# Optimization experiments

Hardware: AMD Instinct MI355X
Metric: run time of the kernel (lower is better)

Reference implementation:

```python
import jax, jax.numpy as jnp
import numpy as np

NEG_INF = -1e9  # matches torch masked_fill value of -1000000000.0


def setup_inputs() -> dict:
    key = jax.random.key(0)
    kq, kk, kv, km = jax.random.split(key, 4)
    B, H, L, D = 4, 16, 1024, 64
    query = jax.random.normal(kq, (B, H, L, D), dtype=jnp.float32)
    k_ = jax.random.normal(kk, (B, H, L, D), dtype=jnp.float32)
    value = jax.random.normal(kv, (B, H, L, D), dtype=jnp.float32)
    mask = jax.random.randint(km, (B, 1, L, L), 0, 2, dtype=jnp.int32)
    return {"query": query, "key": k_, "value": value, "mask": mask}


def reference(query, key, value, mask):
    # scores: [B, H, Lq, Lk]
    d = query.shape[-1]
    scores = jnp.einsum("bhqd,bhkd->bhqk", query, key) / jnp.sqrt(jnp.float32(d))
    masked = mask == 0  # broadcast [B,1,Lq,Lk] over heads
    scores = jnp.where(masked, jnp.float32(NEG_INF), scores)
    p_attn = jax.nn.softmax(scores, axis=-1)
    p_attn = jnp.where(masked, jnp.float32(0.0), p_attn)
    out = jnp.einsum("bhqk,bhkd->bhqd", p_attn, value)
    return out, p_attn
```

## Files before the change

### kernel.cpp

```cpp
#include <hip/hip_runtime.h>
#include <math.h>

typedef __attribute__((ext_vector_type(8))) short short8;
typedef __attribute__((ext_vector_type(4))) float f32x4;

#define NB 4
#define NH 16
#define SL 1024
#define DH 64
#define BQ 64
#define WQ 16
#define KTL 32
#define NT 256
#define NKT (SL / KTL)

#define TILE_SH (2 * KTL * DH)
#define HEAD_SH ((size_t)NKT * TILE_SH)
#define BLOB_SH ((size_t)NB * NH * HEAD_SH)
#define BMROW   (SL / 32)

#define QSCALE 0.18033688011111543f
#define NEGB  -1.5e9f

#if __has_builtin(__builtin_amdgcn_exp2f)
#define EXP2F(x) __builtin_amdgcn_exp2f(x)
#else
#define EXP2F(x) exp2f(x)
#endif

__device__ __forceinline__ unsigned short bf_rne(float x) {
    unsigned int u = __float_as_uint(x);
    u += 0x7fffu + ((u >> 16) & 1u);
    return (unsigned short)(u >> 16);
}
__device__ __forceinline__ void bf_split(float x, unsigned short& h, unsigned short& l) {
    unsigned int u = __float_as_uint(x);
    h = (unsigned short)(u >> 16);
    float r = x - __uint_as_float(u & 0xffff0000u);
    l = bf_rne(r);
}

typedef const __attribute__((address_space(1))) unsigned int guint_t;
typedef __attribute__((address_space(3))) unsigned int luint_t;
__device__ __forceinline__ void gload_lds16(const void* g, void* l) {
    __builtin_amdgcn_global_load_lds((guint_t*)g, (luint_t*)l, 16, 0, 0);
}

#define MFMA(a, b, c) __builtin_amdgcn_mfma_f32_16x16x32_bf16(a, b, c, 0, 0, 0)

#define WAITVM(N) do { asm volatile("s_waitcnt vmcnt(" #N ")" ::: "memory"); \
                       __builtin_amdgcn_sched_barrier(0); } while (0)
#define BAR() do { __builtin_amdgcn_sched_barrier(0); __builtin_amdgcn_s_barrier(); \
                   __builtin_amdgcn_sched_barrier(0); } while (0)
#define SCHED_FENCE() __builtin_amdgcn_sched_barrier(0)

__global__ __launch_bounds__(NT, 4) void prep_mask(
    const int* __restrict__ M, unsigned* __restrict__ bm)
{
    const size_t total = (size_t)NB * SL * SL;
    const int l = threadIdx.x & 63;
    for (size_t i = (size_t)blockIdx.x * NT + threadIdx.x; i < total;
         i += (size_t)gridDim.x * NT) {
        int v = M[i];
        unsigned long long b = __ballot(v != 0);
        if (l == 0)       bm[i >> 5] = (unsigned)b;
        else if (l == 32) bm[i >> 5] = (unsigned)(b >> 32);
    }
}

__global__ __launch_bounds__(NT, 4) void prep_split(
    const float* __restrict__ K, const float* __restrict__ V,
    unsigned short* __restrict__ kb, unsigned short* __restrict__ vb)
{
    __shared__ float sVs[KTL][DH + 4];

    const int t = threadIdx.x;
    const int kt = blockIdx.x, h = blockIdx.y, b = blockIdx.z;
    const size_t goff = (size_t)(b * NH + h) * SL * DH + (size_t)kt * KTL * DH;
    const size_t tks = (size_t)(b * NH + h) * HEAD_SH + (size_t)kt * TILE_SH;

    {
        int kr = t >> 3, c8 = t & 7;
        const float* src = K + goff + kr * DH + c8 * 8;
        float4 a = *(const float4*)src;
        float4 bb = *(const float4*)(src + 4);
        float vals[8] = {a.x, a.y, a.z, a.w, bb.x, bb.y, bb.z, bb.w};
        unsigned int ph[4], pl[4];
        #pragma unroll
        for (int j = 0; j < 4; ++j) {
            unsigned short h0, l0, h1, l1;
            bf_split(vals[2 * j], h0, l0);
            bf_split(vals[2 * j + 1], h1, l1);
            ph[j] = (unsigned int)h0 | ((unsigned int)h1 << 16);
            pl[j] = (unsigned int)l0 | ((unsigned int)l1 << 16);
        }
        int dsw = (c8 * 8) ^ ((kr & 7) << 3);
        *(uint4*)&kb[tks + kr * DH + dsw]           = make_uint4(ph[0], ph[1], ph[2], ph[3]);
        *(uint4*)&kb[tks + KTL * DH + kr * DH + dsw] = make_uint4(pl[0], pl[1], pl[2], pl[3]);
    }

    #pragma unroll
    for (int u = 0; u < 2; ++u) {
        int i = u * NT + t;
        float4 v = *(const float4*)(V + goff + (size_t)i * 4);
        *(float4*)&sVs[i >> 4][(i & 15) * 4] = v;
    }
    __syncthreads();
    {
        int d = t >> 2, k8 = t & 3;
        float vals[8];
        #pragma unroll
        for (int j = 0; j < 8; ++j) vals[j] = sVs[k8 * 8 + j][d];
        unsigned int ph[4], pl[4];
        #pragma unroll
        for (int j = 0; j < 4; ++j) {
            unsigned short h0, l0, h1, l1;
            bf_split(vals[2 * j], h0, l0);
            bf_split(vals[2 * j + 1], h1, l1);
            ph[j] = (unsigned int)h0 | ((unsigned int)h1 << 16);
            pl[j] = (unsigned int)l0 | ((unsigned int)l1 << 16);
        }
        int ksw = (k8 * 8) ^ ((d & 3) << 3);
        *(uint4*)&vb[tks + d * KTL + ksw]            = make_uint4(ph[0], ph[1], ph[2], ph[3]);
        *(uint4*)&vb[tks + KTL * DH + d * KTL + ksw] = make_uint4(pl[0], pl[1], pl[2], pl[3]);
    }
}

__global__ __launch_bounds__(NT, 4) void attn_main(
    const float* __restrict__ Q, const unsigned* __restrict__ bm,
    const unsigned short* __restrict__ kb, const unsigned short* __restrict__ vb,
    float* __restrict__ O, float* __restrict__ P)
{
    __shared__ unsigned short sK[2][TILE_SH];
    __shared__ unsigned short sV[2][TILE_SH];
    __shared__ unsigned short sPh[4][WQ][KTL];
    __shared__ unsigned short sPl[4][WQ][KTL];

    const int t = threadIdx.x;
    const int l = t & 63;
    const int w = __builtin_amdgcn_readfirstlane(t >> 6);
    const int lg = l >> 4, lr = l & 15;

    const int flat = blockIdx.x + (blockIdx.y << 4) + (blockIdx.z << 8);
    const int nid = (flat & 7) * 128 + (flat >> 3);
    const int qt = nid & 15;
    const int hh_ = (nid >> 4) & 15;
    const int b = nid >> 8;
    const int qb = qt * BQ + w * WQ;

    const size_t hoff = (size_t)(b * NH + hh_) * SL * DH;
    const size_t headsh = (size_t)(b * NH + hh_) * HEAD_SH;
    const unsigned short* kbh = kb + headsh;
    const unsigned short* vbh = vb + headsh;
    const unsigned* bmRow = bm + ((size_t)b * SL + qb + lr) * BMROW;
    float* Pw = P + ((size_t)(b * NH + hh_) * SL + qb) * SL;
    float* Ow = O + hoff + (size_t)qb * DH;

    short8 qhi[2], qlo[2];
    {
        const float* src0 = Q + hoff + (size_t)(qb + lr) * DH + lg * 8;
        #pragma unroll
        for (int ds = 0; ds < 2; ++ds) {
            const float* src = src0 + ds * 32;
            float4 a = *(const float4*)src;
            float4 bb = *(const float4*)(src + 4);
            float vals[8] = {a.x, a.y, a.z, a.w, bb.x, bb.y, bb.z, bb.w};
            #pragma unroll
            for (int j = 0; j < 8; ++j) {
                unsigned short hv, lv;
                bf_split(vals[j] * QSCALE, hv, lv);
                qhi[ds][j] = (short)hv;
                qlo[ds][j] = (short)lv;
            }
        }
    }

    auto stage = [&](unsigned short* lds, const unsigned short* gtile) {
        #pragma unroll
        for (int u = 0; u < 2; ++u) {
            const int c = w * 2 + u;
            gload_lds16((const char*)gtile + c * 1024 + l * 16, (char*)lds + c * 1024);
        }
    };

    stage(sK[0], kbh);
    unsigned bmv = bmRow[0];
    float m = -INFINITY, sum = 0.f;
    int cur = 0;

    for (int kt = 0; kt < NKT; ++kt) {
        WAITVM(0);
        BAR();
        unsigned bmn = 0;
        if (kt + 1 < NKT) {
            stage(sK[cur ^ 1], kbh + (size_t)(kt + 1) * TILE_SH);
            bmn = bmRow[kt + 1];
        }
        SCHED_FENCE();

        f32x4 acc[2];
        #pragma unroll
        for (int st = 0; st < 2; ++st) {
            const int krow = st * 16 + lr;
            const int sw = (krow & 7) << 3;
            f32x4 c = {0.f, 0.f, 0.f, 0.f};
            #pragma unroll
            for (int ds = 0; ds < 2; ++ds) {
                int dc = (ds * 32 + lg * 8) ^ sw;
                short8 ah = *(const short8*)&sK[cur][krow * DH + dc];
                short8 al = *(const short8*)&sK[cur][KTL * DH + krow * DH + dc];
                c = MFMA(ah, qhi[ds], c);
                c = MFMA(ah, qlo[ds], c);
                c = MFMA(al, qhi[ds], c);
            }
            acc[st] = c;
        }

        float s[8];
        #pragma unroll
        for (int st = 0; st < 2; ++st)
            #pragma unroll
            for (int j = 0; j < 4; ++j) {
                unsigned bit = (bmv >> (st * 16 + lg * 4 + j)) & 1u;
                s[st * 4 + j] = acc[st][j] + (bit ? 0.f : NEGB);
            }
        float tmax = s[0];
        #pragma unroll
        for (int j = 1; j < 8; ++j) tmax = fmaxf(tmax, s[j]);
        tmax = fmaxf(tmax, __shfl_xor(tmax, 16));
        tmax = fmaxf(tmax, __shfl_xor(tmax, 32));
        const float mn = fmaxf(m, tmax);
        float ts = 0.f;
        #pragma unroll
        for (int j = 0; j < 8; ++j) ts += EXP2F(s[j] - mn);
        ts += __shfl_xor(ts, 16);
        ts += __shfl_xor(ts, 32);
        sum = sum * EXP2F(m - mn) + ts;
        m = mn;
        bmv = bmn;
        cur ^= 1;
    }

    stage(sK[0], kbh);
    stage(sV[0], vbh);
    bmv = bmRow[0];
    const float m2 = m + __log2f(sum);
    f32x4 oacc[4];
    #pragma unroll
    for (int mt = 0; mt < 4; ++mt) oacc[mt] = (f32x4){0.f, 0.f, 0.f, 0.f};
    cur = 0;

    for (int kt = 0; kt < NKT; ++kt) {
        const int k0 = kt * KTL;
        if (kt == 0) { WAITVM(0); } else { WAITVM(2); }
        BAR();
        unsigned bmn = 0;
        if (kt + 1 < NKT) {
            stage(sK[cur ^ 1], kbh + (size_t)(kt + 1) * TILE_SH);
            stage(sV[cur ^ 1], vbh + (size_t)(kt + 1) * TILE_SH);
            bmn = bmRow[kt + 1];
        }
        SCHED_FENCE();

        f32x4 acc[2];
        #pragma unroll
        for (int st = 0; st < 2; ++st) {
            const int krow = st * 16 + lr;
            const int sw = (krow & 7) << 3;
            f32x4 c = {0.f, 0.f, 0.f, 0.f};
            #pragma unroll
            for (int ds = 0; ds < 2; ++ds) {
                int dc = (ds * 32 + lg * 8) ^ sw;
                short8 ah = *(const short8*)&sK[cur][krow * DH + dc];
                short8 al = *(const short8*)&sK[cur][KTL * DH + krow * DH + dc];
                c = MFMA(ah, qhi[ds], c);
                c = MFMA(ah, qlo[ds], c);
                c = MFMA(al, qhi[ds], c);
            }
            acc[st] = c;
        }

        #pragma unroll
        for (int st = 0; st < 2; ++st) {
            float p[4];
            #pragma unroll
            for (int j = 0; j < 4; ++j) {
                unsigned bit = (bmv >> (st * 16 + lg * 4 + j)) & 1u;
                float sj = acc[st][j] + (bit ? 0.f : NEGB);
                p[j] = EXP2F(sj - m2);
            }
            *(float4*)(Pw + (size_t)lr * SL + (k0 + st * 16 + lg * 4)) =
                make_float4(p[0], p[1], p[2], p[3]);
            unsigned short hv[4], lv[4];
            #pragma unroll
            for (int j = 0; j < 4; ++j) bf_split(p[j], hv[j], lv[j]);
            int col = (st * 16 + lg * 4) ^ ((lr & 3) << 3);
            uint2 uh, ul;
            uh.x = (unsigned int)hv[0] | ((unsigned int)hv[1] << 16);
            uh.y = (unsigned int)hv[2] | ((unsigned int)hv[3] << 16);
            ul.x = (unsigned int)lv[0] | ((unsigned int)lv[1] << 16);
            ul.y = (unsigned int)lv[2] | ((unsigned int)lv[3] << 16);
            *(uint2*)&sPh[w][lr][col] = uh;
            *(uint2*)&sPl[w][lr][col] = ul;
        }

        const int pcol = (lg * 8) ^ ((lr & 3) << 3);
        short8 pbh = *(const short8*)&sPh[w][lr][pcol];
        short8 pbl = *(const short8*)&sPl[w][lr][pcol];
        #pragma unroll
        for (int mt = 0; mt < 4; ++mt) {
            const int d = mt * 16 + lr;
            const int col = (lg * 8) ^ ((d & 3) << 3);
            short8 vh = *(const short8*)&sV[cur][d * KTL + col];
            short8 vl = *(const short8*)&sV[cur][KTL * DH + d * KTL + col];
            oacc[mt] = MFMA(vh, pbh, oacc[mt]);
            oacc[mt] = MFMA(vh, pbl, oacc[mt]);
            oacc[mt] = MFMA(vl, pbh, oacc[mt]);
        }
        bmv = bmn;
        cur ^= 1;
    }

    #pragma unroll
    for (int mt = 0; mt < 4; ++mt) {
        float4 o = make_float4(oacc[mt][0], oacc[mt][1], oacc[mt][2], oacc[mt][3]);
        *(float4*)(Ow + (size_t)lr * DH + mt * 16 + lg * 4) = o;
    }
}

__global__ __launch_bounds__(NT, 2) void attn_fallback(
    const float* __restrict__ Q, const float* __restrict__ K,
    const float* __restrict__ V, const int* __restrict__ M,
    float* __restrict__ O, float* __restrict__ P)
{
    __shared__ unsigned short sKhi[64][DH];
    __shared__ unsigned short sKlo[64][DH];
    __shared__ unsigned short sVhi[DH][64];
    __shared__ unsigned short sVlo[DH][64];
    __shared__ unsigned short sPhi[4][WQ][64];
    __shared__ unsigned short sPlo[4][WQ][64];

    const int t = threadIdx.x;
    const int l = t & 63;
    const int w = t >> 6;
    const int lg = l >> 4;
    const int lr = l & 15;

    const int hh_ = blockIdx.y, b = blockIdx.z;
    const int qb = blockIdx.x * BQ + w * WQ;

    const size_t hoff = (size_t)(b * NH + hh_) * SL * DH;
    const float* Kh = K + hoff;
    const float* Vh = V + hoff;
    const int*   Mw = M + ((size_t)b * SL + qb) * SL;
    float*       Pw = P + ((size_t)(b * NH + hh_) * SL + qb) * SL;
    float*       Ow = O + hoff + (size_t)qb * DH;

    short8 qhi[2], qlo[2];
    {
        const float* src0 = Q + hoff + (size_t)(qb + lr) * DH + lg * 8;
        #pragma unroll
        for (int ds = 0; ds < 2; ++ds) {
            const float* src = src0 + ds * 32;
            float4 a = *(const float4*)src;
            float4 bb = *(const float4*)(src + 4);
            float vals[8] = {a.x, a.y, a.z, a.w, bb.x, bb.y, bb.z, bb.w};
            #pragma unroll
            for (int j = 0; j < 8; ++j) {
                unsigned short hv, lv;
                bf_split(vals[j] * 0.125f, hv, lv);
                qhi[ds][j] = (short)hv;
                qlo[ds][j] = (short)lv;
            }
        }
    }

    auto stageK = [&](int k0) {
        #pragma unroll
        for (int u = 0; u < 2; ++u) {
            int idx = u * NT + t;
            int kr = idx >> 3;
            int dc = (idx & 7) * 8;
            const float* src = Kh + (size_t)(k0 + kr) * DH + dc;
            float4 a = *(const float4*)src;
            float4 bb = *(const float4*)(src + 4);
            float vals[8] = {a.x, a.y, a.z, a.w, bb.x, bb.y, bb.z, bb.w};
            unsigned int ph[4], pl[4];
            #pragma unroll
            for (int j = 0; j < 4; ++j) {
                unsigned short h0, l0, h1, l1;
                bf_split(vals[2 * j], h0, l0);
                bf_split(vals[2 * j + 1], h1, l1);
                ph[j] = (unsigned int)h0 | ((unsigned int)h1 << 16);
                pl[j] = (unsigned int)l0 | ((unsigned int)l1 << 16);
            }
            int dsw = dc ^ ((kr & 7) << 3);
            *(uint4*)&sKhi[kr][dsw] = make_uint4(ph[0], ph[1], ph[2], ph[3]);
            *(uint4*)&sKlo[kr][dsw] = make_uint4(pl[0], pl[1], pl[2], pl[3]);
        }
    };

    float m = -INFINITY, sum = 0.f;
    for (int kt = 0; kt < 16; ++kt) {
        const int k0 = kt * 64;
        __syncthreads();
        stageK(k0);
        __syncthreads();
        f32x4 acc[4];
        #pragma unroll
        for (int st = 0; st < 4; ++st) {
            const int krow = st * 16 + lr;
            const int sw = (krow & 7) << 3;
            f32x4 c = {0.f, 0.f, 0.f, 0.f};
            #pragma unroll
            for (int ds = 0; ds < 2; ++ds) {
                int dc = (ds * 32 + lg * 8) ^ sw;
                short8 ah = *(const short8*)&sKhi[krow][dc];
                short8 al = *(const short8*)&sKlo[krow][dc];
                c = MFMA(ah, qhi[ds], c);
                c = MFMA(ah, qlo[ds], c);
                c = MFMA(al, qhi[ds], c);
            }
            acc[st] = c;
        }
        float s[16];
        #pragma unroll
        for (int st = 0; st < 4; ++st) {
            const int4 mv = *(const int4*)(Mw + (size_t)lr * SL + k0 + st * 16 + lg * 4);
            s[st * 4 + 0] = mv.x ? acc[st][0] : -1e9f;
            s[st * 4 + 1] = mv.y ? acc[st][1] : -1e9f;
            s[st * 4 + 2] = mv.z ? acc[st][2] : -1e9f;
            s[st * 4 + 3] = mv.w ? acc[st][3] : -1e9f;
        }
        float tmax = s[0];
        #pragma unroll
        for (int j = 1; j < 16; ++j) tmax = fmaxf(tmax, s[j]);
        tmax = fmaxf(tmax, __shfl_xor(tmax, 16));
        tmax = fmaxf(tmax, __shfl_xor(tmax, 32));
        const float mn = fmaxf(m, tmax);
        float ts = 0.f;
        #pragma unroll
        for (int j = 0; j < 16; ++j) ts += __expf(s[j] - mn);
        ts += __shfl_xor(ts, 16);
        ts += __shfl_xor(ts, 32);
        sum = sum * __expf(m - mn) + ts;
        m = mn;
    }
    const float inv = 1.f / sum;

    f32x4 oacc[4];
    #pragma unroll
    for (int mt = 0; mt < 4; ++mt) oacc[mt] = (f32x4){0.f, 0.f, 0.f, 0.f};

    for (int kt = 0; kt < 16; ++kt) {
        const int k0 = kt * 64;
        __syncthreads();
        stageK(k0);
        {
            int d0 = (t & 15) * 4;
            int kl0 = (t >> 4) * 4;
            float4 r[4];
            #pragma unroll
            for (int i = 0; i < 4; ++i)
                r[i] = *(const float4*)(Vh + (size_t)(k0 + kl0 + i) * DH + d0);
            const float* rp = (const float*)r;
            #pragma unroll
            for (int j = 0; j < 4; ++j) {
                unsigned short hv[4], lv[4];
                #pragma unroll
                for (int i = 0; i < 4; ++i) bf_split(rp[i * 4 + j], hv[i], lv[i]);
                int d = d0 + j;
                int csw = kl0 ^ ((d & 7) << 3);
                uint2 uh, ul;
                uh.x = (unsigned int)hv[0] | ((unsigned int)hv[1] << 16);
                uh.y = (unsigned int)hv[2] | ((unsigned int)hv[3] << 16);
                ul.x = (unsigned int)lv[0] | ((unsigned int)lv[1] << 16);
                ul.y = (unsigned int)lv[2] | ((unsigned int)lv[3] << 16);
                *(uint2*)&sVhi[d][csw] = uh;
                *(uint2*)&sVlo[d][csw] = ul;
            }
        }
        __syncthreads();

        #pragma unroll
        for (int st = 0; st < 4; ++st) {
            const int krow = st * 16 + lr;
            const int sw = (krow & 7) << 3;
            f32x4 c = {0.f, 0.f, 0.f, 0.f};
            #pragma unroll
            for (int ds = 0; ds < 2; ++ds) {
                int dc = (ds * 32 + lg * 8) ^ sw;
                short8 ah = *(const short8*)&sKhi[krow][dc];
                short8 al = *(const short8*)&sKlo[krow][dc];
                c = MFMA(ah, qhi[ds], c);
                c = MFMA(ah, qlo[ds], c);
                c = MFMA(al, qhi[ds], c);
            }
            const int4 mv = *(const int4*)(Mw + (size_t)lr * SL + k0 + st * 16 + lg * 4);
            float p0 = mv.x ? __expf(c[0] - m) * inv : 0.f;
            float p1 = mv.y ? __expf(c[1] - m) * inv : 0.f;
            float p2 = mv.z ? __expf(c[2] - m) * inv : 0.f;
            float p3 = mv.w ? __expf(c[3] - m) * inv : 0.f;
            *(float4*)(Pw + (size_t)lr * SL + (k0 + st * 16 + lg * 4)) =
                make_float4(p0, p1, p2, p3);
            unsigned short hv[4], lv[4];
            bf_split(p0, hv[0], lv[0]);
            bf_split(p1, hv[1], lv[1]);
            bf_split(p2, hv[2], lv[2]);
            bf_split(p3, hv[3], lv[3]);
            int col = (st * 16 + lg * 4) ^ ((lr & 7) << 3);
            uint2 uh, ul;
            uh.x = (unsigned int)hv[0] | ((unsigned int)hv[1] << 16);
            uh.y = (unsigned int)hv[2] | ((unsigned int)hv[3] << 16);
            ul.x = (unsigned int)lv[0] | ((unsigned int)lv[1] << 16);
            ul.y = (unsigned int)lv[2] | ((unsigned int)lv[3] << 16);
            *(uint2*)&sPhi[w][lr][col] = uh;
            *(uint2*)&sPlo[w][lr][col] = ul;
        }

        short8 pbh[2], pbl[2];
        #pragma unroll
        for (int ks = 0; ks < 2; ++ks) {
            int col = (ks * 32 + lg * 8) ^ ((lr & 7) << 3);
            pbh[ks] = *(const short8*)&sPhi[w][lr][col];
            pbl[ks] = *(const short8*)&sPlo[w][lr][col];
        }
        #pragma unroll
        for (int mt = 0; mt < 4; ++mt) {
            const int d = mt * 16 + lr;
            const int swd = (d & 7) << 3;
            #pragma unroll
            for (int ks = 0; ks < 2; ++ks) {
                int col = (ks * 32 + lg * 8) ^ swd;
                short8 vh = *(const short8*)&sVhi[d][col];
                short8 vl = *(const short8*)&sVlo[d][col];
                oacc[mt] = MFMA(vh, pbh[ks], oacc[mt]);
                oacc[mt] = MFMA(vh, pbl[ks], oacc[mt]);
                oacc[mt] = MFMA(vl, pbh[ks], oacc[mt]);
            }
        }
    }

    #pragma unroll
    for (int mt = 0; mt < 4; ++mt) {
        float4 o = make_float4(oacc[mt][0], oacc[mt][1], oacc[mt][2], oacc[mt][3]);
        *(float4*)(Ow + (size_t)lr * DH + mt * 16 + lg * 4) = o;
    }
}

extern "C" void kernel_launch(void* const* d_in, const int* in_sizes, int n_in,
                              void* d_out, int out_size, void* d_ws, size_t ws_size,
                              hipStream_t stream) {
    const float* Q = (const float*)d_in[0];
    const float* K = (const float*)d_in[1];
    const float* V = (const float*)d_in[2];
    const int*   M = (const int*)d_in[3];
    float* O = (float*)d_out;
    float* P = O + (size_t)NB * NH * SL * DH;

    const size_t bm_dw = (size_t)NB * SL * BMROW;
    const size_t need = bm_dw * 4 + 2 * BLOB_SH * 2;
    if (ws_size >= need) {
        unsigned* bmp = (unsigned*)d_ws;
        unsigned short* kbp = (unsigned short*)(bmp + bm_dw);
        unsigned short* vbp = kbp + BLOB_SH;
        hipLaunchKernelGGL(prep_mask, dim3(1024, 1, 1), dim3(NT, 1, 1), 0, stream, M, bmp);
        hipLaunchKernelGGL(prep_split, dim3(NKT, NH, NB), dim3(NT, 1, 1), 0, stream,
                           K, V, kbp, vbp);
        hipLaunchKernelGGL(attn_main, dim3(SL / BQ, NH, NB), dim3(NT, 1, 1), 0, stream,
                           Q, bmp, kbp, vbp, O, P);
    } else {
        hipLaunchKernelGGL(attn_fallback, dim3(SL / BQ, NH, NB), dim3(NT, 1, 1), 0, stream,
                           Q, K, V, M, O, P);
    }
}
```

Measured before the change: 156.1 us.

## Pre-swizzle K/V into MFMA fragment order and load directly from global

The prep kernel now writes K and V tiles in per-lane MFMA fragment order, so the attention kernel loads operand fragments straight from global memory into registers. This drops the LDS double-buffering, the async global-to-LDS copies, and the per-tile barriers. P and O stores become nontemporal to avoid polluting cache. The trade is losing LDS sharing across the four waves, which now each fetch the same K/V tiles from L1/L2, and losing the explicit prefetch overlap, which now depends on the compiler and the unroll-by-2.

Result: slower. 180.2 us (+15.4%).

```diff
diff --git a/kernel.cpp b/kernel.cpp
--- a/kernel.cpp
+++ b/kernel.cpp
@@ -14,7 +14,7 @@
 #define NT 256
 #define NKT (SL / KTL)
 
-#define TILE_SH (2 * KTL * DH)
+#define TILE_SH 4096
 #define HEAD_SH ((size_t)NKT * TILE_SH)
 #define BLOB_SH ((size_t)NB * NH * HEAD_SH)
 #define BMROW   (SL / 32)
@@ -40,19 +40,7 @@
     l = bf_rne(r);
 }
 
-typedef const __attribute__((address_space(1))) unsigned int guint_t;
-typedef __attribute__((address_space(3))) unsigned int luint_t;
-__device__ __forceinline__ void gload_lds16(const void* g, void* l) {
-    __builtin_amdgcn_global_load_lds((guint_t*)g, (luint_t*)l, 16, 0, 0);
-}
-
 #define MFMA(a, b, c) __builtin_amdgcn_mfma_f32_16x16x32_bf16(a, b, c, 0, 0, 0)
-
-#define WAITVM(N) do { asm volatile("s_waitcnt vmcnt(" #N ")" ::: "memory"); \
-                       __builtin_amdgcn_sched_barrier(0); } while (0)
-#define BAR() do { __builtin_amdgcn_sched_barrier(0); __builtin_amdgcn_s_barrier(); \
-                   __builtin_amdgcn_sched_barrier(0); } while (0)
-#define SCHED_FENCE() __builtin_amdgcn_sched_barrier(0)
 
 __global__ __launch_bounds__(NT, 4) void prep_mask(
     const int* __restrict__ M, unsigned* __restrict__ bm)
@@ -94,9 +82,10 @@
             ph[j] = (unsigned int)h0 | ((unsigned int)h1 << 16);
             pl[j] = (unsigned int)l0 | ((unsigned int)l1 << 16);
         }
-        int dsw = (c8 * 8) ^ ((kr & 7) << 3);
-        *(uint4*)&kb[tks + kr * DH + dsw]           = make_uint4(ph[0], ph[1], ph[2], ph[3]);
-        *(uint4*)&kb[tks + KTL * DH + kr * DH + dsw] = make_uint4(pl[0], pl[1], pl[2], pl[3]);
+        const int st = kr >> 4, lr = kr & 15, ds = c8 >> 2, lg = c8 & 3;
+        const int l = lg * 16 + lr, c = st * 2 + ds;
+        *(uint4*)&kb[tks + c * 512 + l * 8]        = make_uint4(ph[0], ph[1], ph[2], ph[3]);
+        *(uint4*)&kb[tks + 2048 + c * 512 + l * 8] = make_uint4(pl[0], pl[1], pl[2], pl[3]);
     }
 
     #pragma unroll
@@ -107,10 +96,12 @@
     }
     __syncthreads();
     {
-        int d = t >> 2, k8 = t & 3;
+        const int mt = t >> 6, l = t & 63;
+        const int d = mt * 16 + (l & 15);
+        const int kbase = (l >> 4) * 8;
         float vals[8];
         #pragma unroll
-        for (int j = 0; j < 8; ++j) vals[j] = sVs[k8 * 8 + j][d];
+        for (int j = 0; j < 8; ++j) vals[j] = sVs[kbase + j][d];
         unsigned int ph[4], pl[4];
         #pragma unroll
         for (int j = 0; j < 4; ++j) {
@@ -120,9 +111,8 @@
             ph[j] = (unsigned int)h0 | ((unsigned int)h1 << 16);
             pl[j] = (unsigned int)l0 | ((unsigned int)l1 << 16);
         }
-        int ksw = (k8 * 8) ^ ((d & 3) << 3);
-        *(uint4*)&vb[tks + d * KTL + ksw]            = make_uint4(ph[0], ph[1], ph[2], ph[3]);
-        *(uint4*)&vb[tks + KTL * DH + d * KTL + ksw] = make_uint4(pl[0], pl[1], pl[2], pl[3]);
+        *(uint4*)&vb[tks + mt * 512 + l * 8]        = make_uint4(ph[0], ph[1], ph[2], ph[3]);
+        *(uint4*)&vb[tks + 2048 + mt * 512 + l * 8] = make_uint4(pl[0], pl[1], pl[2], pl[3]);
     }
 }
 
@@ -131,8 +121,6 @@
     const unsigned short* __restrict__ kb, const unsigned short* __restrict__ vb,
     float* __restrict__ O, float* __restrict__ P)
 {
-    __shared__ unsigned short sK[2][TILE_SH];
-    __shared__ unsigned short sV[2][TILE_SH];
     __shared__ unsigned short sPh[4][WQ][KTL];
     __shared__ unsigned short sPl[4][WQ][KTL];
 
@@ -175,43 +163,31 @@
         }
     }
 
-    auto stage = [&](unsigned short* lds, const unsigned short* gtile) {
-        #pragma unroll
-        for (int u = 0; u < 2; ++u) {
-            const int c = w * 2 + u;
-            gload_lds16((const char*)gtile + c * 1024 + l * 16, (char*)lds + c * 1024);
-        }
-    };
-
-    stage(sK[0], kbh);
-    unsigned bmv = bmRow[0];
     float m = -INFINITY, sum = 0.f;
-    int cur = 0;
-
+
+    #pragma unroll 2
     for (int kt = 0; kt < NKT; ++kt) {
-        WAITVM(0);
-        BAR();
-        unsigned bmn = 0;
-        if (kt + 1 < NKT) {
-            stage(sK[cur ^ 1], kbh + (size_t)(kt + 1) * TILE_SH);
-            bmn = bmRow[kt + 1];
-        }
-        SCHED_FENCE();
+        const unsigned short* tb = kbh + (size_t)kt * TILE_SH;
+        const unsigned bmv = bmRow[kt];
+        short8 ah[2][2], al[2][2];
+        #pragma unroll
+        for (int st = 0; st < 2; ++st)
+            #pragma unroll
+            for (int ds = 0; ds < 2; ++ds) {
+                const int c = st * 2 + ds;
+                ah[st][ds] = *(const short8*)(tb + c * 512 + l * 8);
+                al[st][ds] = *(const short8*)(tb + 2048 + c * 512 + l * 8);
+            }
 
         f32x4 acc[2];
         #pragma unroll
         for (int st = 0; st < 2; ++st) {
-            const int krow = st * 16 + lr;
-            const int sw = (krow & 7) << 3;
             f32x4 c = {0.f, 0.f, 0.f, 0.f};
             #pragma unroll
             for (int ds = 0; ds < 2; ++ds) {
-                int dc = (ds * 32 + lg * 8) ^ sw;
-                short8 ah = *(const short8*)&sK[cur][krow * DH + dc];
-                short8 al = *(const short8*)&sK[cur][KTL * DH + krow * DH + dc];
-                c = MFMA(ah, qhi[ds], c);
-                c = MFMA(ah, qlo[ds], c);
-                c = MFMA(al, qhi[ds], c);
+                c = MFMA(ah[st][ds], qhi[ds], c);
+                c = MFMA(ah[st][ds], qlo[ds], c);
+                c = MFMA(al[st][ds], qhi[ds], c);
             }
             acc[st] = c;
         }
@@ -237,47 +213,47 @@
         ts += __shfl_xor(ts, 32);
         sum = sum * EXP2F(m - mn) + ts;
         m = mn;
-        bmv = bmn;
-        cur ^= 1;
-    }
-
-    stage(sK[0], kbh);
-    stage(sV[0], vbh);
-    bmv = bmRow[0];
+    }
+
     const float m2 = m + __log2f(sum);
     f32x4 oacc[4];
     #pragma unroll
     for (int mt = 0; mt < 4; ++mt) oacc[mt] = (f32x4){0.f, 0.f, 0.f, 0.f};
-    cur = 0;
 
     for (int kt = 0; kt < NKT; ++kt) {
         const int k0 = kt * KTL;
-        if (kt == 0) { WAITVM(0); } else { WAITVM(2); }
-        BAR();
-        unsigned bmn = 0;
-        if (kt + 1 < NKT) {
-            stage(sK[cur ^ 1], kbh + (size_t)(kt + 1) * TILE_SH);
-            stage(sV[cur ^ 1], vbh + (size_t)(kt + 1) * TILE_SH);
-            bmn = bmRow[kt + 1];
-        }
-        SCHED_FENCE();
+        const unsigned short* tbK = kbh + (size_t)kt * TILE_SH;
+        const unsigned short* tbV = vbh + (size_t)kt * TILE_SH;
+        const unsigned bmv = bmRow[kt];
+
+        short8 ah[2][2], al[2][2];
+        #pragma unroll
+        for (int st = 0; st < 2; ++st)
+            #pragma unroll
+            for (int ds = 0; ds < 2; ++ds) {
+                const int c = st * 2 + ds;
+                ah[st][ds] = *(const short8*)(tbK + c * 512 + l * 8);
+                al[st][ds] = *(const short8*)(tbK + 2048 + c * 512 + l * 8);
+            }
 
         f32x4 acc[2];
         #pragma unroll
         for (int st = 0; st < 2; ++st) {
-            const int krow = st * 16 + lr;
-            const int sw = (krow & 7) << 3;
             f32x4 c = {0.f, 0.f, 0.f, 0.f};
             #pragma unroll
             for (int ds = 0; ds < 2; ++ds) {
-                int dc = (ds * 32 + lg * 8) ^ sw;
-                short8 ah = *(const short8*)&sK[cur][krow * DH + dc];
-                short8 al = *(const short8*)&sK[cur][KTL * DH + krow * DH + dc];
-                c = MFMA(ah, qhi[ds], c);
-                c = MFMA(ah, qlo[ds], c);
-                c = MFMA(al, qhi[ds], c);
+                c = MFMA(ah[st][ds], qhi[ds], c);
+                c = MFMA(ah[st][ds], qlo[ds], c);
+                c = MFMA(al[st][ds], qhi[ds], c);
             }
             acc[st] = c;
+        }
+
+        short8 vh[4], vl[4];
+        #pragma unroll
+        for (int mt = 0; mt < 4; ++mt) {
+            vh[mt] = *(const short8*)(tbV + mt * 512 + l * 8);
+            vl[mt] = *(const short8*)(tbV + 2048 + mt * 512 + l * 8);
         }
 
         #pragma unroll
@@ -289,8 +265,9 @@
                 float sj = acc[st][j] + (bit ? 0.f : NEGB);
                 p[j] = EXP2F(sj - m2);
             }
-            *(float4*)(Pw + (size_t)lr * SL + (k0 + st * 16 + lg * 4)) =
-                make_float4(p[0], p[1], p[2], p[3]);
+            f32x4 pv4 = {p[0], p[1], p[2], p[3]};
+            __builtin_nontemporal_store(
+                pv4, (f32x4*)(Pw + (size_t)lr * SL + (k0 + st * 16 + lg * 4)));
             unsigned short hv[4], lv[4];
             #pragma unroll
             for (int j = 0; j < 4; ++j) bf_split(p[j], hv[j], lv[j]);
@@ -309,22 +286,16 @@
         short8 pbl = *(const short8*)&sPl[w][lr][pcol];
         #pragma unroll
         for (int mt = 0; mt < 4; ++mt) {
-            const int d = mt * 16 + lr;
-            const int col = (lg * 8) ^ ((d & 3) << 3);
-            short8 vh = *(const short8*)&sV[cur][d * KTL + col];
-            short8 vl = *(const short8*)&sV[cur][KTL * DH + d * KTL + col];
-            oacc[mt] = MFMA(vh, pbh, oacc[mt]);
-            oacc[mt] = MFMA(vh, pbl, oacc[mt]);
-            oacc[mt] = MFMA(vl, pbh, oacc[mt]);
-        }
-        bmv = bmn;
-        cur ^= 1;
+            oacc[mt] = MFMA(vh[mt], pbh, oacc[mt]);
+            oacc[mt] = MFMA(vh[mt], pbl, oacc[mt]);
+            oacc[mt] = MFMA(vl[mt], pbh, oacc[mt]);
+        }
     }
 
     #pragma unroll
     for (int mt = 0; mt < 4; ++mt) {
-        float4 o = make_float4(oacc[mt][0], oacc[mt][1], oacc[mt][2], oacc[mt][3]);
-        *(float4*)(Ow + (size_t)lr * DH + mt * 16 + lg * 4) = o;
+        __builtin_nontemporal_store(
+            oacc[mt], (f32x4*)(Ow + (size_t)lr * DH + mt * 16 + lg * 4));
     }
 }
 
```

## Drop bf16 hi/lo split and use single bf16 MFMAs with nontemporal stores

Applied to the files above, without the earlier changes.

Replaces the three-term split-bf16 emulation of fp32 matmuls with plain bf16 operands for Q, K, V and P. This cuts MFMA count, LDS reads, the preprocessed K/V blob size and the staging loads per tile to a third or a half. The P and O stores become nontemporal to reduce cache pollution from the large probability write. The risk is reduced numerical accuracy relative to the fp32 reference.

Result: slower. 160.5 us (+2.8%).

```diff
diff --git a/kernel.cpp b/kernel.cpp
--- a/kernel.cpp
+++ b/kernel.cpp
@@ -14,7 +14,7 @@
 #define NT 256
 #define NKT (SL / KTL)
 
-#define TILE_SH (2 * KTL * DH)
+#define TILE_SH (KTL * DH)
 #define HEAD_SH ((size_t)NKT * TILE_SH)
 #define BLOB_SH ((size_t)NB * NH * HEAD_SH)
 #define BMROW   (SL / 32)
@@ -85,18 +85,13 @@
         float4 a = *(const float4*)src;
         float4 bb = *(const float4*)(src + 4);
         float vals[8] = {a.x, a.y, a.z, a.w, bb.x, bb.y, bb.z, bb.w};
-        unsigned int ph[4], pl[4];
-        #pragma unroll
-        for (int j = 0; j < 4; ++j) {
-            unsigned short h0, l0, h1, l1;
-            bf_split(vals[2 * j], h0, l0);
-            bf_split(vals[2 * j + 1], h1, l1);
-            ph[j] = (unsigned int)h0 | ((unsigned int)h1 << 16);
-            pl[j] = (unsigned int)l0 | ((unsigned int)l1 << 16);
-        }
+        unsigned int pk[4];
+        #pragma unroll
+        for (int j = 0; j < 4; ++j)
+            pk[j] = (unsigned int)bf_rne(vals[2 * j]) |
+                    ((unsigned int)bf_rne(vals[2 * j + 1]) << 16);
         int dsw = (c8 * 8) ^ ((kr & 7) << 3);
-        *(uint4*)&kb[tks + kr * DH + dsw]           = make_uint4(ph[0], ph[1], ph[2], ph[3]);
-        *(uint4*)&kb[tks + KTL * DH + kr * DH + dsw] = make_uint4(pl[0], pl[1], pl[2], pl[3]);
+        *(uint4*)&kb[tks + kr * DH + dsw] = make_uint4(pk[0], pk[1], pk[2], pk[3]);
     }
 
     #pragma unroll
@@ -111,18 +106,13 @@
         float vals[8];
         #pragma unroll
         for (int j = 0; j < 8; ++j) vals[j] = sVs[k8 * 8 + j][d];
-        unsigned int ph[4], pl[4];
-        #pragma unroll
-        for (int j = 0; j < 4; ++j) {
-            unsigned short h0, l0, h1, l1;
-            bf_split(vals[2 * j], h0, l0);
-            bf_split(vals[2 * j + 1], h1, l1);
-            ph[j] = (unsigned int)h0 | ((unsigned int)h1 << 16);
-            pl[j] = (unsigned int)l0 | ((unsigned int)l1 << 16);
-        }
+        unsigned int pk[4];
+        #pragma unroll
+        for (int j = 0; j < 4; ++j)
+            pk[j] = (unsigned int)bf_rne(vals[2 * j]) |
+                    ((unsigned int)bf_rne(vals[2 * j + 1]) << 16);
         int ksw = (k8 * 8) ^ ((d & 3) << 3);
-        *(uint4*)&vb[tks + d * KTL + ksw]            = make_uint4(ph[0], ph[1], ph[2], ph[3]);
-        *(uint4*)&vb[tks + KTL * DH + d * KTL + ksw] = make_uint4(pl[0], pl[1], pl[2], pl[3]);
+        *(uint4*)&vb[tks + d * KTL + ksw] = make_uint4(pk[0], pk[1], pk[2], pk[3]);
     }
 }
 
@@ -134,7 +124,6 @@
     __shared__ unsigned short sK[2][TILE_SH];
     __shared__ unsigned short sV[2][TILE_SH];
     __shared__ unsigned short sPh[4][WQ][KTL];
-    __shared__ unsigned short sPl[4][WQ][KTL];
 
     const int t = threadIdx.x;
     const int l = t & 63;
@@ -156,7 +145,7 @@
     float* Pw = P + ((size_t)(b * NH + hh_) * SL + qb) * SL;
     float* Ow = O + hoff + (size_t)qb * DH;
 
-    short8 qhi[2], qlo[2];
+    short8 qf[2];
     {
         const float* src0 = Q + hoff + (size_t)(qb + lr) * DH + lg * 8;
         #pragma unroll
@@ -166,22 +155,16 @@
             float4 bb = *(const float4*)(src + 4);
             float vals[8] = {a.x, a.y, a.z, a.w, bb.x, bb.y, bb.z, bb.w};
             #pragma unroll
-            for (int j = 0; j < 8; ++j) {
-                unsigned short hv, lv;
-                bf_split(vals[j] * QSCALE, hv, lv);
-                qhi[ds][j] = (short)hv;
-                qlo[ds][j] = (short)lv;
-            }
+            for (int j = 0; j < 8; ++j)
+                qf[ds][j] = (short)bf_rne(vals[j] * QSCALE);
         }
     }
 
     auto stage = [&](unsigned short* lds, const unsigned short* gtile) {
-        #pragma unroll
-        for (int u = 0; u < 2; ++u) {
-            const int c = w * 2 + u;
-            gload_lds16((const char*)gtile + c * 1024 + l * 16, (char*)lds + c * 1024);
-        }
+        gload_lds16((const char*)gtile + w * 1024 + l * 16, (char*)lds + w * 1024);
     };
+
+    const f32x4 zero = {0.f, 0.f, 0.f, 0.f};
 
     stage(sK[0], kbh);
     unsigned bmv = bmRow[0];
@@ -203,15 +186,12 @@
         for (int st = 0; st < 2; ++st) {
             const int krow = st * 16 + lr;
             const int sw = (krow & 7) << 3;
-            f32x4 c = {0.f, 0.f, 0.f, 0.f};
+            f32x4 c = zero;
             #pragma unroll
             for (int ds = 0; ds < 2; ++ds) {
                 int dc = (ds * 32 + lg * 8) ^ sw;
-                short8 ah = *(const short8*)&sK[cur][krow * DH + dc];
-                short8 al = *(const short8*)&sK[cur][KTL * DH + krow * DH + dc];
-                c = MFMA(ah, qhi[ds], c);
-                c = MFMA(ah, qlo[ds], c);
-                c = MFMA(al, qhi[ds], c);
+                short8 af = *(const short8*)&sK[cur][krow * DH + dc];
+                c = MFMA(af, qf[ds], c);
             }
             acc[st] = c;
         }
@@ -247,7 +227,7 @@
     const float m2 = m + __log2f(sum);
     f32x4 oacc[4];
     #pragma unroll
-    for (int mt = 0; mt < 4; ++mt) oacc[mt] = (f32x4){0.f, 0.f, 0.f, 0.f};
+    for (int mt = 0; mt < 4; ++mt) oacc[mt] = zero;
     cur = 0;
 
     for (int kt = 0; kt < NKT; ++kt) {
@@ -267,15 +247,12 @@
         for (int st = 0; st < 2; ++st) {
             const int krow = st * 16 + lr;
             const int sw = (krow & 7) << 3;
-            f32x4 c = {0.f, 0.f, 0.f, 0.f};
+            f32x4 c = zero;
             #pragma unroll
             for (int ds = 0; ds < 2; ++ds) {
                 int dc = (ds * 32 + lg * 8) ^ sw;
-                short8 ah = *(const short8*)&sK[cur][krow * DH + dc];
-                short8 al = *(const short8*)&sK[cur][KTL * DH + krow * DH + dc];
-                c = MFMA(ah, qhi[ds], c);
-                c = MFMA(ah, qlo[ds], c);
-                c = MFMA(al, qhi[ds], c);
+                short8 af = *(const short8*)&sK[cur][krow * DH + dc];
+                c = MFMA(af, qf[ds], c);
             }
             acc[st] = c;
         }
@@ -289,33 +266,24 @@
                 float sj = acc[st][j] + (bit ? 0.f : NEGB);
                 p[j] = EXP2F(sj - m2);
             }
-            *(float4*)(Pw + (size_t)lr * SL + (k0 + st * 16 + lg * 4)) =
-                make_float4(p[0], p[1], p[2], p[3]);
-            unsigned short hv[4], lv[4];
-            #pragma unroll
-            for (int j = 0; j < 4; ++j) bf_split(p[j], hv[j], lv[j]);
+            f32x4 pv4 = {p[0], p[1], p[2], p[3]};
+            __builtin_nontemporal_store(
+                pv4, (f32x4*)(Pw + (size_t)lr * SL + (k0 + st * 16 + lg * 4)));
             int col = (st * 16 + lg * 4) ^ ((lr & 3) << 3);
-            uint2 uh, ul;
-            uh.x = (unsigned int)hv[0] | ((unsigned int)hv[1] << 16);
-            uh.y = (unsigned int)hv[2] | ((unsigned int)hv[3] << 16);
-            ul.x = (unsigned int)lv[0] | ((unsigned int)lv[1] << 16);
-            ul.y = (unsigned int)lv[2] | ((unsigned int)lv[3] << 16);
+            uint2 uh;
+            uh.x = (unsigned int)bf_rne(p[0]) | ((unsigned int)bf_rne(p[1]) << 16);
+            uh.y = (unsigned int)bf_rne(p[2]) | ((unsigned int)bf_rne(p[3]) << 16);
             *(uint2*)&sPh[w][lr][col] = uh;
-            *(uint2*)&sPl[w][lr][col] = ul;
         }
 
         const int pcol = (lg * 8) ^ ((lr & 3) << 3);
-        short8 pbh = *(const short8*)&sPh[w][lr][pcol];
-        short8 pbl = *(const short8*)&sPl[w][lr][pcol];
+        short8 pb = *(const short8*)&sPh[w][lr][pcol];
         #pragma unroll
         for (int mt = 0; mt < 4; ++mt) {
             const int d = mt * 16 + lr;
             const int col = (lg * 8) ^ ((d & 3) << 3);
-            short8 vh = *(const short8*)&sV[cur][d * KTL + col];
-            short8 vl = *(const short8*)&sV[cur][KTL * DH + d * KTL + col];
-            oacc[mt] = MFMA(vh, pbh, oacc[mt]);
-            oacc[mt] = MFMA(vh, pbl, oacc[mt]);
-            oacc[mt] = MFMA(vl, pbh, oacc[mt]);
+            short8 vf = *(const short8*)&sV[cur][d * KTL + col];
+            oacc[mt] = MFMA(vf, pb, oacc[mt]);
         }
         bmv = bmn;
         cur ^= 1;
@@ -323,8 +291,8 @@
 
     #pragma unroll
     for (int mt = 0; mt < 4; ++mt) {
-        float4 o = make_float4(oacc[mt][0], oacc[mt][1], oacc[mt][2], oacc[mt][3]);
-        *(float4*)(Ow + (size_t)lr * DH + mt * 16 + lg * 4) = o;
+        __builtin_nontemporal_store(
+            oacc[mt], (f32x4*)(Ow + (size_t)lr * DH + mt * 16 + lg * 4));
     }
 }
 
```
